# Kernel tuning notes

Hardware: AMD Instinct MI355X
Metric: run time of the kernel (lower is better)

The kernel has to match this reference:

```python
import jax, jax.numpy as jnp
import numpy as np

DIM = 4096
N_HEADS = 32
N_KV = 8
HEAD_DIM = 128
BATCH = 32
CACHE_LEN = 2048 + 128  # hard-coded in init_kv_cache
START_POS = 2047
ROPE_BASE = 10000.0


def setup_inputs() -> dict:
    key = jax.random.key(0)
    ks = jax.random.split(key, 5)
    qkv_dim = (N_HEADS + 2 * N_KV) * HEAD_DIM  # fused QKV width
    return {
        "x": jax.random.normal(ks[0], (BATCH, DIM), jnp.float32) * 0.02,
        "wqkv": jax.random.normal(ks[1], (DIM, qkv_dim), jnp.float32) * 0.02,
        "wo": jax.random.normal(ks[2], (DIM, DIM), jnp.float32) * 0.02,
        "cache_k": jax.random.normal(ks[3], (BATCH, N_KV, CACHE_LEN, HEAD_DIM), jnp.float32) * 0.02,
        "cache_v": jax.random.normal(ks[4], (BATCH, N_KV, CACHE_LEN, HEAD_DIM), jnp.float32) * 0.02,
        "start_pos": START_POS,
    }


def _rope_cos_sin(pos):
    # Llama half-split RoPE; equivalent to the head_dim x head_dim rotation matrix
    half = HEAD_DIM // 2
    inv_freq = 1.0 / (ROPE_BASE ** (jnp.arange(half, dtype=jnp.float32) * 2.0 / HEAD_DIM))
    ang = pos * inv_freq
    cos = jnp.concatenate([jnp.cos(ang), jnp.cos(ang)])
    sin = jnp.concatenate([jnp.sin(ang), jnp.sin(ang)])
    return cos, sin


def _rotate_half(t):
    h = t.shape[-1] // 2
    return jnp.concatenate([-t[..., h:], t[..., :h]], axis=-1)


def reference(x, wqkv, wo, cache_k, cache_v, start_pos):
    scale = 1.0 / np.sqrt(HEAD_DIM)
    n_rep = N_HEADS // N_KV

    # fused QKV projection
    qkv = x @ wqkv  # (B, (H + 2*K) * D)
    q = qkv[:, : N_HEADS * HEAD_DIM].reshape(BATCH, N_KV, n_rep, HEAD_DIM)
    k = qkv[:, N_HEADS * HEAD_DIM : (N_HEADS + N_KV) * HEAD_DIM].reshape(BATCH, N_KV, HEAD_DIM)
    v = qkv[:, (N_HEADS + N_KV) * HEAD_DIM :].reshape(BATCH, N_KV, HEAD_DIM)

    # RoPE at position start_pos (rotation-matrix form in the original)
    cos, sin = _rope_cos_sin(jnp.float32(start_pos))
    q = q * cos + _rotate_half(q) * sin
    k = k * cos + _rotate_half(k) * sin

    # KV cache update at start_pos
    cache_k = cache_k.at[:, :, start_pos, :].set(k)
    cache_v = cache_v.at[:, :, start_pos, :].set(v)

    # grouped-query attention over the whole (masked) cache
    scores = jnp.einsum("bgrd,bgsd->bgrs", q, cache_k) * scale  # (B, KV, rep, S)
    valid = jnp.arange(CACHE_LEN) <= start_pos
    scores = jnp.where(valid[None, None, None, :], scores, jnp.float32(-1e9))
    probs = jax.nn.softmax(scores, axis=-1)
    attn = jnp.einsum("bgrs,bgsd->bgrd", probs, cache_v).reshape(BATCH, DIM)

    # output projection
    return attn @ wo
```

## Files before the change

### kernel.cpp

```cpp
#include <hip/hip_runtime.h>
#include <math.h>

#define DIM 4096
#define NH 32
#define NKV 8
#define HD 128
#define BATCH 32
#define CL 2176
#define QKV_DIM 6144
#define NREP 4

template<int N>
__global__ void gemm_partial(const float* __restrict__ x, const float* __restrict__ w,
                             float* __restrict__ part) {
    __shared__ float xs[128 * 36];
    const int t = threadIdx.x;
    const int n0 = blockIdx.x * 256;
    const int k0 = blockIdx.y * 128;

    for (int i = 0; i < 16; ++i) {
        int e = t + i * 256;
        int b = e >> 7;
        int kk = e & 127;
        xs[kk * 36 + b] = x[(size_t)b * DIM + k0 + kk];
    }
    __syncthreads();

    float acc[32];
#pragma unroll
    for (int b = 0; b < 32; ++b) acc[b] = 0.f;

    const float* wp = w + (size_t)k0 * N + n0 + t;
    for (int kk = 0; kk < 128; ++kk) {
        float wv = wp[(size_t)kk * N];
        const float4* xr = (const float4*)&xs[kk * 36];
#pragma unroll
        for (int b4 = 0; b4 < 8; ++b4) {
            float4 xv = xr[b4];
            acc[b4 * 4 + 0] += xv.x * wv;
            acc[b4 * 4 + 1] += xv.y * wv;
            acc[b4 * 4 + 2] += xv.z * wv;
            acc[b4 * 4 + 3] += xv.w * wv;
        }
    }

    float* pp = part + (size_t)blockIdx.y * 32 * N + n0 + t;
#pragma unroll
    for (int b = 0; b < 32; ++b) pp[(size_t)b * N] = acc[b];
}

__global__ void qkv_finish(const float* __restrict__ part, const int* __restrict__ sp_p,
                           float* __restrict__ fin) {
    const int b = blockIdx.x, h = blockIdx.y, d = threadIdx.x;
    const int sp = *sp_p;
    const int col = h * 128 + d;

    float s = 0.f;
    for (int kc = 0; kc < 32; ++kc)
        s += part[(size_t)kc * 32 * QKV_DIM + (size_t)b * QKV_DIM + col];

    __shared__ float v[128];
    float outv = s;
    if (h < 40) {
        v[d] = s;
        __syncthreads();
        int j = d & 63;
        float inv_freq = powf(10000.0f, -(float)(2 * j) / 128.0f);
        float ang = (float)sp * inv_freq;
        float c = cosf(ang), sn = sinf(ang);
        float rot = (d < 64) ? -v[d + 64] : v[d - 64];
        outv = s * c + rot * sn;
    }
    fin[((size_t)b * 48 + h) * 128 + d] = outv;
}

__global__ void attn_scores(const float* __restrict__ fin, const float* __restrict__ cache_k,
                            const int* __restrict__ sp_p, float* __restrict__ scores) {
    const int bg = blockIdx.x;
    const int b = bg >> 3, g = bg & 7;
    const int sp = *sp_p;
    const int t = threadIdx.x;
    const int w = t >> 6, lane = t & 63, sl = lane & 31, half = lane >> 5;

    float4 qf[4];
#pragma unroll
    for (int h = 0; h < 4; ++h)
        qf[h] = *(const float4*)(fin + ((size_t)b * 48 + g * 4 + h) * 128 + sl * 4);

    const float scale = 0.08838834764831845f;
    const float* kbase = cache_k + ((size_t)b * NKV + g) * CL * HD;
    const float* knew = fin + ((size_t)b * 48 + 32 + g) * 128;

    const int s_begin = blockIdx.y * 1088;
    const int s_end = s_begin + 1088;

    for (int i = s_begin + w * 2; i < s_end; i += 32) {
        int s = i + half;
        const float* krow = (s == sp) ? knew : (kbase + (size_t)s * HD);
        float4 kv = *(const float4*)(krow + sl * 4);

        float p[4];
#pragma unroll
        for (int h = 0; h < 4; ++h)
            p[h] = qf[h].x * kv.x + qf[h].y * kv.y + qf[h].z * kv.z + qf[h].w * kv.w;

#pragma unroll
        for (int off = 1; off < 32; off <<= 1) {
#pragma unroll
            for (int h = 0; h < 4; ++h) p[h] += __shfl_xor(p[h], off);
        }

        if (sl == 0) {
            bool valid = (s <= sp);
            float4 sc;
            sc.x = valid ? p[0] * scale : -1e9f;
            sc.y = valid ? p[1] * scale : -1e9f;
            sc.z = valid ? p[2] * scale : -1e9f;
            sc.w = valid ? p[3] * scale : -1e9f;
            *(float4*)(scores + ((size_t)bg * CL + s) * 4) = sc;
        }
    }
}

__global__ void softmax_k(float* __restrict__ scores) {
    const int bg = blockIdx.x, h = blockIdx.y, t = threadIdx.x;
    float* sb = scores + (size_t)bg * CL * 4 + h;

    float vals[9];
    float m = -1e30f;
#pragma unroll
    for (int i = 0; i < 9; ++i) {
        int s = t + i * 256;
        vals[i] = (s < CL) ? sb[(size_t)s * 4] : -1e30f;
        m = fmaxf(m, vals[i]);
    }
#pragma unroll
    for (int off = 1; off < 64; off <<= 1) m = fmaxf(m, __shfl_xor(m, off));
    __shared__ float redm[4];
    const int w = t >> 6, lane = t & 63;
    if (lane == 0) redm[w] = m;
    __syncthreads();
    m = fmaxf(fmaxf(redm[0], redm[1]), fmaxf(redm[2], redm[3]));

    float l = 0.f;
#pragma unroll
    for (int i = 0; i < 9; ++i) {
        float e = expf(vals[i] - m);
        vals[i] = e;
        l += e;
    }
#pragma unroll
    for (int off = 1; off < 64; off <<= 1) l += __shfl_xor(l, off);
    __shared__ float redl[4];
    if (lane == 0) redl[w] = l;
    __syncthreads();
    l = redl[0] + redl[1] + redl[2] + redl[3];

    float inv = 1.f / l;
#pragma unroll
    for (int i = 0; i < 9; ++i) {
        int s = t + i * 256;
        if (s < CL) sb[(size_t)s * 4] = vals[i] * inv;
    }
}

__global__ void attn_pv(const float* __restrict__ scores, const float* __restrict__ cache_v,
                        const float* __restrict__ fin, const int* __restrict__ sp_p,
                        float* __restrict__ attn) {
    const int bg = blockIdx.x;
    const int b = bg >> 3, g = bg & 7;
    const int sp = *sp_p;
    const int t = threadIdx.x;
    const int grp = t >> 5, sl = t & 31;

    const float* vbase = cache_v + ((size_t)b * NKV + g) * CL * HD;
    const float* vnew = fin + ((size_t)b * 48 + 40 + g) * 128;
    const float* pb = scores + (size_t)bg * CL * 4;

    float o[4][4];
#pragma unroll
    for (int h = 0; h < 4; ++h)
#pragma unroll
        for (int c = 0; c < 4; ++c) o[h][c] = 0.f;

    for (int s = grp; s < CL; s += 32) {
        const float* vrow = (s == sp) ? vnew : (vbase + (size_t)s * HD);
        float4 vv = *(const float4*)(vrow + sl * 4);
        float4 pp = *(const float4*)(pb + (size_t)s * 4);
        o[0][0] += pp.x * vv.x; o[0][1] += pp.x * vv.y; o[0][2] += pp.x * vv.z; o[0][3] += pp.x * vv.w;
        o[1][0] += pp.y * vv.x; o[1][1] += pp.y * vv.y; o[1][2] += pp.y * vv.z; o[1][3] += pp.y * vv.w;
        o[2][0] += pp.z * vv.x; o[2][1] += pp.z * vv.y; o[2][2] += pp.z * vv.z; o[2][3] += pp.z * vv.w;
        o[3][0] += pp.w * vv.x; o[3][1] += pp.w * vv.y; o[3][2] += pp.w * vv.z; o[3][3] += pp.w * vv.w;
    }

    __shared__ float red[32 * 512];
#pragma unroll
    for (int h = 0; h < 4; ++h)
        *(float4*)&red[grp * 512 + h * 128 + sl * 4] = make_float4(o[h][0], o[h][1], o[h][2], o[h][3]);
    __syncthreads();

    for (int step = 16; step >= 1; step >>= 1) {
        if (grp < step) {
#pragma unroll
            for (int i = 0; i < 16; ++i) {
                int j = sl + i * 32;
                red[grp * 512 + j] += red[(grp + step) * 512 + j];
            }
        }
        __syncthreads();
    }

    if (t < 512) {
        int h = t >> 7, d = t & 127;
        attn[(size_t)b * DIM + (g * 4 + h) * 128 + d] = red[h * 128 + d];
    }
}

__global__ void out_reduce(const float* __restrict__ part, float* __restrict__ out) {
    const int e = blockIdx.x * 256 + threadIdx.x;
    float s = 0.f;
    for (int kc = 0; kc < 32; ++kc) s += part[(size_t)kc * 32 * DIM + e];
    out[e] = s;
}

extern "C" void kernel_launch(void* const* d_in, const int* in_sizes, int n_in,
                              void* d_out, int out_size, void* d_ws, size_t ws_size,
                              hipStream_t stream) {
    const float* x       = (const float*)d_in[0];
    const float* wqkv    = (const float*)d_in[1];
    const float* wo      = (const float*)d_in[2];
    const float* cache_k = (const float*)d_in[3];
    const float* cache_v = (const float*)d_in[4];
    const int*   sp      = (const int*)d_in[5];
    float* out = (float*)d_out;
    float* ws  = (float*)d_ws;

    float* part1  = ws;
    float* fin    = part1 + 6291456;
    float* scores = fin + 196608;
    float* attn   = scores + 2228224;
    float* part2  = attn + 131072;

    gemm_partial<QKV_DIM><<<dim3(24, 32), 256, 0, stream>>>(x, wqkv, part1);
    qkv_finish<<<dim3(32, 48), 128, 0, stream>>>(part1, sp, fin);
    attn_scores<<<dim3(256, 2), 1024, 0, stream>>>(fin, cache_k, sp, scores);
    softmax_k<<<dim3(256, 4), 256, 0, stream>>>(scores);
    attn_pv<<<256, 1024, 0, stream>>>(scores, cache_v, fin, sp, attn);
    gemm_partial<DIM><<<dim3(16, 32), 256, 0, stream>>>(attn, wo, part2);
    out_reduce<<<512, 256, 0, stream>>>(part2, out);
}
```

Before: 735.1 us.

## Read GEMM activations directly, restripe score kernel per head, vectorize softmax over heads

The GEMM kernel drops its shared-memory staging of x and instead reads the activation values straight from global memory, relying on caches and unrolling. The score kernel now gives each wave one query head and a stripe of key rows, with four lanes per key row and a two-step shuffle reduction. It runs one block per batch-group instead of two, so K rows are read four times, once per head. Softmax handles all four heads in one block using float4 loads and reductions, replacing four separate strided passes.

```diff
diff --git a/kernel.cpp b/kernel.cpp
--- a/kernel.cpp
+++ b/kernel.cpp
@@ -13,35 +13,22 @@
 template<int N>
 __global__ void gemm_partial(const float* __restrict__ x, const float* __restrict__ w,
                              float* __restrict__ part) {
-    __shared__ float xs[128 * 36];
     const int t = threadIdx.x;
     const int n0 = blockIdx.x * 256;
     const int k0 = blockIdx.y * 128;
 
-    for (int i = 0; i < 16; ++i) {
-        int e = t + i * 256;
-        int b = e >> 7;
-        int kk = e & 127;
-        xs[kk * 36 + b] = x[(size_t)b * DIM + k0 + kk];
-    }
-    __syncthreads();
-
     float acc[32];
 #pragma unroll
     for (int b = 0; b < 32; ++b) acc[b] = 0.f;
 
     const float* wp = w + (size_t)k0 * N + n0 + t;
+    const float* xp = x + k0;
+#pragma unroll 4
     for (int kk = 0; kk < 128; ++kk) {
         float wv = wp[(size_t)kk * N];
-        const float4* xr = (const float4*)&xs[kk * 36];
-#pragma unroll
-        for (int b4 = 0; b4 < 8; ++b4) {
-            float4 xv = xr[b4];
-            acc[b4 * 4 + 0] += xv.x * wv;
-            acc[b4 * 4 + 1] += xv.y * wv;
-            acc[b4 * 4 + 2] += xv.z * wv;
-            acc[b4 * 4 + 3] += xv.w * wv;
-        }
+#pragma unroll
+        for (int b = 0; b < 32; ++b)
+            acc[b] += xp[(size_t)b * DIM + kk] * wv;
     }
 
     float* pp = part + (size_t)blockIdx.y * 32 * N + n0 + t;
@@ -74,99 +61,118 @@
     fin[((size_t)b * 48 + h) * 128 + d] = outv;
 }
 
-__global__ void attn_scores(const float* __restrict__ fin, const float* __restrict__ cache_k,
-                            const int* __restrict__ sp_p, float* __restrict__ scores) {
+__global__ __launch_bounds__(1024) void attn_scores(
+        const float* __restrict__ fin, const float* __restrict__ cache_k,
+        const int* __restrict__ sp_p, float* __restrict__ scores) {
     const int bg = blockIdx.x;
     const int b = bg >> 3, g = bg & 7;
     const int sp = *sp_p;
     const int t = threadIdx.x;
-    const int w = t >> 6, lane = t & 63, sl = lane & 31, half = lane >> 5;
-
-    float4 qf[4];
-#pragma unroll
-    for (int h = 0; h < 4; ++h)
-        qf[h] = *(const float4*)(fin + ((size_t)b * 48 + g * 4 + h) * 128 + sl * 4);
+    const int wave = t >> 6, lane = t & 63;
+    const int h = wave & 3, stripe = wave >> 2;
+    const int sq = lane >> 2, dq = lane & 3;
+
+    const float* qrow = fin + ((size_t)b * 48 + g * 4 + h) * 128;
+    float4 qv[8];
+#pragma unroll
+    for (int i = 0; i < 8; ++i)
+        qv[i] = *(const float4*)(qrow + dq * 4 + i * 16);
 
     const float scale = 0.08838834764831845f;
     const float* kbase = cache_k + ((size_t)b * NKV + g) * CL * HD;
     const float* knew = fin + ((size_t)b * 48 + 32 + g) * 128;
 
-    const int s_begin = blockIdx.y * 1088;
-    const int s_end = s_begin + 1088;
-
-    for (int i = s_begin + w * 2; i < s_end; i += 32) {
-        int s = i + half;
+    const int s_begin = stripe * 544;
+    for (int s0 = s_begin; s0 < s_begin + 544; s0 += 16) {
+        const int s = s0 + sq;
         const float* krow = (s == sp) ? knew : (kbase + (size_t)s * HD);
-        float4 kv = *(const float4*)(krow + sl * 4);
-
-        float p[4];
-#pragma unroll
-        for (int h = 0; h < 4; ++h)
-            p[h] = qf[h].x * kv.x + qf[h].y * kv.y + qf[h].z * kv.z + qf[h].w * kv.w;
-
-#pragma unroll
-        for (int off = 1; off < 32; off <<= 1) {
-#pragma unroll
-            for (int h = 0; h < 4; ++h) p[h] += __shfl_xor(p[h], off);
-        }
-
-        if (sl == 0) {
-            bool valid = (s <= sp);
-            float4 sc;
-            sc.x = valid ? p[0] * scale : -1e9f;
-            sc.y = valid ? p[1] * scale : -1e9f;
-            sc.z = valid ? p[2] * scale : -1e9f;
-            sc.w = valid ? p[3] * scale : -1e9f;
-            *(float4*)(scores + ((size_t)bg * CL + s) * 4) = sc;
-        }
+        float p = 0.f;
+#pragma unroll
+        for (int i = 0; i < 8; ++i) {
+            float4 kv = *(const float4*)(krow + dq * 4 + i * 16);
+            p += qv[i].x * kv.x + qv[i].y * kv.y + qv[i].z * kv.z + qv[i].w * kv.w;
+        }
+        p += __shfl_xor(p, 1);
+        p += __shfl_xor(p, 2);
+        if (dq == 0)
+            scores[((size_t)bg * CL + s) * 4 + h] = (s <= sp) ? p * scale : -1e9f;
     }
 }
 
 __global__ void softmax_k(float* __restrict__ scores) {
-    const int bg = blockIdx.x, h = blockIdx.y, t = threadIdx.x;
-    float* sb = scores + (size_t)bg * CL * 4 + h;
-
-    float vals[9];
-    float m = -1e30f;
+    const int bg = blockIdx.x, t = threadIdx.x;
+    float4* sb = (float4*)(scores + (size_t)bg * CL * 4);
+
+    float4 vals[9];
+    float4 m = make_float4(-1e30f, -1e30f, -1e30f, -1e30f);
 #pragma unroll
     for (int i = 0; i < 9; ++i) {
         int s = t + i * 256;
-        vals[i] = (s < CL) ? sb[(size_t)s * 4] : -1e30f;
-        m = fmaxf(m, vals[i]);
-    }
-#pragma unroll
-    for (int off = 1; off < 64; off <<= 1) m = fmaxf(m, __shfl_xor(m, off));
-    __shared__ float redm[4];
+        if (s < CL) {
+            vals[i] = sb[s];
+            m.x = fmaxf(m.x, vals[i].x); m.y = fmaxf(m.y, vals[i].y);
+            m.z = fmaxf(m.z, vals[i].z); m.w = fmaxf(m.w, vals[i].w);
+        } else {
+            vals[i] = make_float4(-1e30f, -1e30f, -1e30f, -1e30f);
+        }
+    }
+#pragma unroll
+    for (int off = 1; off < 64; off <<= 1) {
+        m.x = fmaxf(m.x, __shfl_xor(m.x, off));
+        m.y = fmaxf(m.y, __shfl_xor(m.y, off));
+        m.z = fmaxf(m.z, __shfl_xor(m.z, off));
+        m.w = fmaxf(m.w, __shfl_xor(m.w, off));
+    }
+    __shared__ float4 redm[4];
     const int w = t >> 6, lane = t & 63;
     if (lane == 0) redm[w] = m;
     __syncthreads();
-    m = fmaxf(fmaxf(redm[0], redm[1]), fmaxf(redm[2], redm[3]));
-
-    float l = 0.f;
+    m.x = fmaxf(fmaxf(redm[0].x, redm[1].x), fmaxf(redm[2].x, redm[3].x));
+    m.y = fmaxf(fmaxf(redm[0].y, redm[1].y), fmaxf(redm[2].y, redm[3].y));
+    m.z = fmaxf(fmaxf(redm[0].z, redm[1].z), fmaxf(redm[2].z, redm[3].z));
+    m.w = fmaxf(fmaxf(redm[0].w, redm[1].w), fmaxf(redm[2].w, redm[3].w));
+
+    float4 l = make_float4(0.f, 0.f, 0.f, 0.f);
 #pragma unroll
     for (int i = 0; i < 9; ++i) {
-        float e = expf(vals[i] - m);
-        vals[i] = e;
-        l += e;
-    }
-#pragma unroll
-    for (int off = 1; off < 64; off <<= 1) l += __shfl_xor(l, off);
-    __shared__ float redl[4];
+        vals[i].x = expf(vals[i].x - m.x);
+        vals[i].y = expf(vals[i].y - m.y);
+        vals[i].z = expf(vals[i].z - m.z);
+        vals[i].w = expf(vals[i].w - m.w);
+        l.x += vals[i].x; l.y += vals[i].y; l.z += vals[i].z; l.w += vals[i].w;
+    }
+#pragma unroll
+    for (int off = 1; off < 64; off <<= 1) {
+        l.x += __shfl_xor(l.x, off);
+        l.y += __shfl_xor(l.y, off);
+        l.z += __shfl_xor(l.z, off);
+        l.w += __shfl_xor(l.w, off);
+    }
+    __shared__ float4 redl[4];
     if (lane == 0) redl[w] = l;
     __syncthreads();
-    l = redl[0] + redl[1] + redl[2] + redl[3];
-
-    float inv = 1.f / l;
+    l.x = redl[0].x + redl[1].x + redl[2].x + redl[3].x;
+    l.y = redl[0].y + redl[1].y + redl[2].y + redl[3].y;
+    l.z = redl[0].z + redl[1].z + redl[2].z + redl[3].z;
+    l.w = redl[0].w + redl[1].w + redl[2].w + redl[3].w;
+
+    float4 inv = make_float4(1.f / l.x, 1.f / l.y, 1.f / l.z, 1.f / l.w);
 #pragma unroll
     for (int i = 0; i < 9; ++i) {
         int s = t + i * 256;
-        if (s < CL) sb[(size_t)s * 4] = vals[i] * inv;
-    }
-}
-
-__global__ void attn_pv(const float* __restrict__ scores, const float* __restrict__ cache_v,
-                        const float* __restrict__ fin, const int* __restrict__ sp_p,
-                        float* __restrict__ attn) {
+        if (s < CL) {
+            float4 o;
+            o.x = vals[i].x * inv.x; o.y = vals[i].y * inv.y;
+            o.z = vals[i].z * inv.z; o.w = vals[i].w * inv.w;
+            sb[s] = o;
+        }
+    }
+}
+
+__global__ __launch_bounds__(1024) void attn_pv(
+        const float* __restrict__ scores, const float* __restrict__ cache_v,
+        const float* __restrict__ fin, const int* __restrict__ sp_p,
+        float* __restrict__ attn) {
     const int bg = blockIdx.x;
     const int b = bg >> 3, g = bg & 7;
     const int sp = *sp_p;
@@ -243,8 +249,8 @@
 
     gemm_partial<QKV_DIM><<<dim3(24, 32), 256, 0, stream>>>(x, wqkv, part1);
     qkv_finish<<<dim3(32, 48), 128, 0, stream>>>(part1, sp, fin);
-    attn_scores<<<dim3(256, 2), 1024, 0, stream>>>(fin, cache_k, sp, scores);
-    softmax_k<<<dim3(256, 4), 256, 0, stream>>>(scores);
+    attn_scores<<<256, 1024, 0, stream>>>(fin, cache_k, sp, scores);
+    softmax_k<<<256, 256, 0, stream>>>(scores);
     attn_pv<<<256, 1024, 0, stream>>>(scores, cache_v, fin, sp, attn);
     gemm_partial<DIM><<<dim3(16, 32), 256, 0, stream>>>(attn, wo, part2);
     out_reduce<<<512, 256, 0, stream>>>(part2, out);
```

After: 779.6 us. 6.0% more time.
